# Performance work log

Hardware: AMD Instinct MI355X
Metric: run time of the kernel (lower is better)

## Reference

```python
import jax, jax.numpy as jnp
import numpy as np

B, C, Np, D = 16, 64, 128, 128
HT = 4      # time heads
HS = 4      # space heads (GAT)
F = D       # GAT out_channels
DK = D // 2 # q/k proj dim
TOPK = 8
NEG = -1e30

def ln(x, g, b):
    m = x.mean(-1, keepdims=True)
    v = jnp.mean((x - m) ** 2, axis=-1, keepdims=True)
    return (x - m) / jnp.sqrt(v + 1e-5) * g + b

def setup_inputs() -> dict:
    key = jax.random.key(0)
    ks = jax.random.split(key, 16)
    w = lambda k, s: (jax.random.normal(k, s, jnp.float32) * 0.02)
    return dict(
        H_in=jax.random.normal(ks[0], (B, C, Np, D), jnp.float32),
        static_adj=jax.random.normal(ks[1], (C, C), jnp.float32) * 0.1,
        attn_in_w=w(ks[2], (3 * D, D)), attn_in_b=jnp.zeros((3 * D,), jnp.float32),
        attn_out_w=w(ks[3], (D, D)), attn_out_b=jnp.zeros((D,), jnp.float32),
        ln1_g=jnp.ones((D,), jnp.float32), ln1_b=jnp.zeros((D,), jnp.float32),
        ln2_g=jnp.ones((D,), jnp.float32), ln2_b=jnp.zeros((D,), jnp.float32),
        ff1_w=w(ks[4], (4 * D, D)), ff1_b=jnp.zeros((4 * D,), jnp.float32),
        ff2_w=w(ks[5], (D, 4 * D)), ff2_b=jnp.zeros((D,), jnp.float32),
        tnorm_g=jnp.ones((D,), jnp.float32), tnorm_b=jnp.zeros((D,), jnp.float32),
        q_w=w(ks[6], (DK, D)), q_b=jnp.zeros((DK,), jnp.float32),
        k_w=w(ks[7], (DK, D)), k_b=jnp.zeros((DK,), jnp.float32),
        gat_w=w(ks[8], (HS, F, D)),
        gat_att_src=w(ks[9], (HS, F)), gat_att_dst=w(ks[10], (HS, F)),
        gat_bias=jnp.zeros((D,), jnp.float32),
        snorm_g=jnp.ones((D,), jnp.float32), snorm_b=jnp.zeros((D,), jnp.float32),
    )

def _forward(H_in, static_adj, attn_in_w, attn_in_b, attn_out_w, attn_out_b,
             ln1_g, ln1_b, ln2_g, ln2_b, ff1_w, ff1_b, ff2_w, ff2_b,
             tnorm_g, tnorm_b, q_w, q_b, k_w, k_b,
             gat_w, gat_att_src, gat_att_dst, gat_bias, snorm_g, snorm_b):
    dh = D // HT
    # ---- temporal transformer encoder layer (norm_first) on [B*C, Np, D]
    x0 = H_in.reshape(B * C, Np, D)
    h = ln(x0, ln1_g, ln1_b)
    qkv = h @ attn_in_w.T + attn_in_b
    q, k, v = jnp.split(qkv, 3, axis=-1)
    q = q.reshape(-1, Np, HT, dh).transpose(0, 2, 1, 3)
    k = k.reshape(-1, Np, HT, dh).transpose(0, 2, 1, 3)
    v = v.reshape(-1, Np, HT, dh).transpose(0, 2, 1, 3)
    att = jax.nn.softmax(jnp.einsum('nhqd,nhkd->nhqk', q, k) / jnp.sqrt(jnp.float32(dh)), axis=-1)
    o = jnp.einsum('nhqk,nhkd->nhqd', att, v).transpose(0, 2, 1, 3).reshape(-1, Np, D)
    x = x0 + (o @ attn_out_w.T + attn_out_b)
    h2 = ln(x, ln2_g, ln2_b)
    x = x + jax.nn.relu(h2 @ ff1_w.T + ff1_b) @ ff2_w.T + ff2_b
    H_temp = ln(x0 + x, tnorm_g, tnorm_b).reshape(B, C, Np, D)
    # ---- dynamic adjacency from temporal summary
    Hs = H_temp.mean(axis=2)                              # [B,C,D]
    q2 = Hs @ q_w.T + q_b
    k2 = Hs @ k_w.T + k_b
    sim = jnp.einsum('bcd,bed->bce', q2, k2) * (DK ** -0.5)
    A = jnp.tanh(sim) + static_adj[None]                  # [B,C,C]
    # ---- top-k edge mask per sample (row r -> its top-k cols, no self loops)
    kk = max(1, min(TOPK, C - 1))
    idx = jax.lax.top_k(A, kk)[1]                         # [B,C,kk]
    mask = jnp.any(jax.nn.one_hot(idx, C, dtype=bool), axis=2)  # [B,C,C]
    mask = mask & (~jnp.eye(C, dtype=bool)) & (A != 0)
    # ---- dense masked GAT over all (B, Np) graphs; src=row, dst=col
    xh = jnp.einsum('bcpd,hfd->bphcf', H_temp, gat_w)     # [B,Np,HS,C,F]
    asrc = jnp.einsum('bphcf,hf->bphc', xh, gat_att_src)
    adst = jnp.einsum('bphcf,hf->bphc', xh, gat_att_dst)
    e = asrc[..., :, None] + adst[..., None, :]           # [B,Np,HS,src,dst]
    e = jnp.where(e > 0, e, 0.2 * e)                      # LeakyReLU(0.2)
    mb = mask[:, None, None, :, :]
    e = jnp.where(mb, e, NEG)
    e = e - e.max(axis=3, keepdims=True)                  # softmax over src per dst
    wgt = jnp.exp(e) * mb
    s = wgt.sum(axis=3, keepdims=True)
    a = wgt / jnp.where(s > 0, s, 1.0)
    out = jnp.einsum('bphst,bphsf->bphtf', a, xh).mean(axis=2) + gat_bias  # [B,Np,C,F]
    out = out.transpose(0, 2, 1, 3)                       # [B,C,Np,D]
    return ln(out + H_temp, snorm_g, snorm_b)

def reference(H_in, static_adj, attn_in_w, attn_in_b, attn_out_w, attn_out_b,
              ln1_g, ln1_b, ln2_g, ln2_b, ff1_w, ff1_b, ff2_w, ff2_b,
              tnorm_g, tnorm_b, q_w, q_b, k_w, k_b,
              gat_w, gat_att_src, gat_att_dst, gat_bias, snorm_g, snorm_b):
    return _forward(H_in, static_adj, attn_in_w, attn_in_b, attn_out_w, attn_out_b,
                    ln1_g, ln1_b, ln2_g, ln2_b, ff1_w, ff1_b, ff2_w, ff2_b,
                    tnorm_g, tnorm_b, q_w, q_b, k_w, k_b,
                    gat_w, gat_att_src, gat_att_dst, gat_bias, snorm_g, snorm_b)
```

## Files before the change

### kernel.cpp

```cpp
#include <hip/hip_runtime.h>
#include <cstdint>


typedef __attribute__((ext_vector_type(8)))  short bf16x8;
typedef __attribute__((ext_vector_type(16))) float f32x16;
#define MFMA32(a, b, c) __builtin_amdgcn_mfma_f32_32x32x16_bf16((a), (b), (c), 0, 0, 0)

__device__ __forceinline__ unsigned short f2bf(float f) {
    unsigned int u = __float_as_uint(f);
    u += 0x7fffu + ((u >> 16) & 1u);
    return (unsigned short)(u >> 16);
}
__device__ __forceinline__ float bf2f(unsigned short u) {
    return __uint_as_float(((unsigned int)u) << 16);
}

__device__ __forceinline__ bf16x8 lds_frag(const unsigned short* p) {
    union { bf16x8 v; ushort4 h[2]; } u;
    u.h[0] = *(const ushort4*)p;
    u.h[1] = *(const ushort4*)(p + 4);
    return u.v;
}
__device__ __forceinline__ bf16x8 gfrag(const unsigned short* p) {
    union { bf16x8 v; uint4 u; } t;
    t.u = *(const uint4*)p;
    return t.v;
}

__device__ __forceinline__ int rowmap(int r, int hl) { return (r & 3) + 8 * (r >> 2) + 4 * hl; }

__device__ __forceinline__ unsigned int pk2(float lo, float hi) {
    return (unsigned int)f2bf(lo) | ((unsigned int)f2bf(hi) << 16);
}

template<int B>
__device__ __forceinline__ bf16x8 pack_frag(const f32x16& p) {
    unsigned int a0 = pk2(p[B + 0], p[B + 1]);
    unsigned int a1 = pk2(p[B + 2], p[B + 3]);
    unsigned int b0 = pk2(p[B + 4], p[B + 5]);
    unsigned int b1 = pk2(p[B + 6], p[B + 7]);
    asm("v_permlane32_swap_b32 %0, %1" : "+v"(b0), "+v"(a0));
    asm("v_permlane32_swap_b32 %0, %1" : "+v"(b1), "+v"(a1));
    union { bf16x8 v; unsigned int w[4]; } u;
    u.w[0] = a0; u.w[1] = a1; u.w[2] = b0; u.w[3] = b1;
    return u.v;
}

__global__ void wconv_kernel(const float* __restrict__ wqkv, const float* __restrict__ wout,
                             const float* __restrict__ w1, const float* __restrict__ w2,
                             const float* __restrict__ gw,
                             unsigned short* __restrict__ dst) {
    int i = blockIdx.x * 256 + threadIdx.x;
    float v;
    if (i < 49152)       v = wqkv[i];
    else if (i < 65536)  v = wout[i - 49152];
    else if (i < 131072) v = w1[i - 65536];
    else if (i < 196608) v = w2[i - 131072];
    else                 v = gw[i - 196608];
    dst[i] = f2bf(v);
}

__global__ void wa_kernel(const float* __restrict__ gw, const float* __restrict__ asw,
                          const float* __restrict__ adw,
                          float* __restrict__ waS, float* __restrict__ waD) {
    int t = blockIdx.x * 256 + threadIdx.x;
    int h = t >> 8, d = (t >> 1) & 127, which = t & 1;
    const float* av = which ? adw : asw;
    float s = 0.f;
    for (int f = 0; f < 128; f++) s += av[h * 128 + f] * gw[(h * 128 + f) * 128 + d];
    (which ? waD : waS)[h * 128 + d] = s;
}

#define QKV_STAGE(H, KBB, VTB) do {                                              \
    f32x16 accq, acck, accv;                                                     \
    _Pragma("unroll") for (int r = 0; r < 16; r++)                               \
        accq[r] = bqkv[(H) * 32 + rowmap(r, hl)];                                \
    float bk_ = bqkv[128 + (H) * 32 + l31];                                      \
    float bv_ = bqkv[256 + (H) * 32 + l31];                                      \
    _Pragma("unroll") for (int r = 0; r < 16; r++) { acck[r] = bk_; accv[r] = bv_; } \
    const unsigned short* wq_ = wqkv_b + ((H) * 32 + l31) * 128 + hl * 8;        \
    const unsigned short* wk_ = wqkv_b + (128 + (H) * 32 + l31) * 128 + hl * 8;  \
    const unsigned short* wv_ = wqkv_b + (256 + (H) * 32 + l31) * 128 + hl * 8;  \
    _Pragma("unroll") for (int k0 = 0; k0 < 128; k0 += 16) {                     \
        bf16x8 a_ = lds_frag(&RA[myrow][k0 + hl * 8]);                           \
        accq = MFMA32(gfrag(wq_ + k0), a_, accq);   \
        acck = MFMA32(a_, gfrag(wk_ + k0), acck);                                \
        accv = MFMA32(a_, gfrag(wv_ + k0), accv);                                \
    }                                                                            \
    _Pragma("unroll") for (int r = 0; r < 16; r++) {                             \
        int tok_ = wv * 32 + rowmap(r, hl);                                      \
        KBB[tok_][l31] = f2bf(acck[r]);                                          \
        VTB[l31][tok_] = f2bf(accv[r]);                                          \
    }                                                                            \
    qf0_ = pack_frag<0>(accq);                                                   \
    qf1_ = pack_frag<8>(accq);                                                   \
} while (0)

#define ATTN_PHASE(H, KBB, VTB, NEXTQKV) do {                                    \
    f32x16 sacc[4];                                                              \
    _Pragma("unroll") for (int t = 0; t < 4; t++)                                \
    _Pragma("unroll") for (int r = 0; r < 16; r++) sacc[t][r] = 0.f;             \
    _Pragma("unroll") for (int t = 0; t < 4; t++) {                              \
        bf16x8 ka0 = lds_frag(&KBB[t * 32 + l31][hl * 8]);                       \
        sacc[t] = MFMA32(ka0, qf0_, sacc[t]);                                    \
        bf16x8 ka1 = lds_frag(&KBB[t * 32 + l31][16 + hl * 8]);                  \
        sacc[t] = MFMA32(ka1, qf1_, sacc[t]);                                    \
    }                                                                            \
    NEXTQKV;                                                                     \
    const float scale_ = 0.17677669529663687f;                   \
    float m0 = -1e30f;                                                           \
    _Pragma("unroll") for (int t = 0; t < 4; t++)                                \
    _Pragma("unroll") for (int r = 0; r < 16; r++) m0 = fmaxf(m0, sacc[t][r]);   \
    m0 = fmaxf(m0, __shfl_xor(m0, 32));                                          \
    float ssum = 0.f;                                                            \
    _Pragma("unroll") for (int t = 0; t < 4; t++)                                \
    _Pragma("unroll") for (int r = 0; r < 16; r++) {                             \
        float e_ = __expf(scale_ * (sacc[t][r] - m0));                           \
        sacc[t][r] = e_; ssum += e_;                                             \
    }                                                                            \
    ssum += __shfl_xor(ssum, 32);                                                \
    float rinv_ = 1.f / ssum;                                                    \
    _Pragma("unroll") for (int t = 0; t < 4; t++)                                \
    _Pragma("unroll") for (int r = 0; r < 16; r++) sacc[t][r] *= rinv_;          \
    f32x16 oacc;                                                                 \
    _Pragma("unroll") for (int r = 0; r < 16; r++) oacc[r] = 0.f;                \
    _Pragma("unroll") for (int t = 0; t < 4; t++) {                              \
        bf16x8 pf0 = pack_frag<0>(sacc[t]);                                      \
        bf16x8 v0_ = lds_frag(&VTB[l31][t * 32 + hl * 8]);                       \
        oacc = MFMA32(pf0, v0_, oacc);                                           \
        bf16x8 pf1 = pack_frag<8>(sacc[t]);                                      \
        bf16x8 v1_ = lds_frag(&VTB[l31][t * 32 + 16 + hl * 8]);                  \
        oacc = MFMA32(pf1, v1_, oacc);                                           \
    }                                                                            \
    _Pragma("unroll") for (int j = 0; j < 8; j++)                                \
        opk[H][j] = pk2(oacc[2*j], oacc[2*j+1]);                                 \
} while (0)

__global__ __launch_bounds__(256, 2)
void temporal_kernel(const float* __restrict__ Hin,
                     const unsigned short* __restrict__ wqkv_b, const float* __restrict__ bqkv,
                     const unsigned short* __restrict__ wout_b, const float* __restrict__ bout,
                     const float* __restrict__ g1, const float* __restrict__ b1,
                     const float* __restrict__ g2, const float* __restrict__ b2,
                     const unsigned short* __restrict__ w1_b, const float* __restrict__ bf1,
                     const unsigned short* __restrict__ w2_b, const float* __restrict__ bf2,
                     const float* __restrict__ tg, const float* __restrict__ tb,
                     float* __restrict__ Htemp, float* __restrict__ Hs) {
    __shared__ unsigned short RA[128][132];
    __shared__ double RBd[4416];
    unsigned short (*kb0)[36]  = (unsigned short(*)[36])RBd;
    unsigned short (*vT0)[132] = (unsigned short(*)[132])((char*)RBd + 9216);
    unsigned short (*kb1)[36]  = (unsigned short(*)[36])((char*)RBd + 17664);
    unsigned short (*vT1)[132] = (unsigned short(*)[132])((char*)RBd + 26880);
    unsigned short (*rscr)[32][36] = (unsigned short(*)[32][36])RBd;
    float (*hsred)[128] = (float(*)[128])((char*)RBd + 9216);

    const int n = blockIdx.x;
    const int tid = threadIdx.x;
    const int lane = tid & 63;
    const int wv = tid >> 6;
    const int hl = lane >> 5;
    const int l31 = lane & 31;
    const int myrow = wv * 32 + l31;

    {
        int row = tid >> 1, hf = tid & 1;
        const float* src = Hin + ((long)n * 128 + row) * 128 + hf * 64;
        float xv[64];
        float s = 0.f, qs = 0.f;
#pragma unroll
        for (int i = 0; i < 64; i += 4) {
            float4 t = *(const float4*)(src + i);
            xv[i] = t.x; xv[i+1] = t.y; xv[i+2] = t.z; xv[i+3] = t.w;
        }
#pragma unroll
        for (int i = 0; i < 64; i++) { s += xv[i]; qs += xv[i] * xv[i]; }
        s += __shfl_xor(s, 1); qs += __shfl_xor(qs, 1);
        float mu = s * 0.0078125f;
        float rs = rsqrtf(fmaxf(qs * 0.0078125f - mu * mu, 0.f) + 1e-5f);
#pragma unroll
        for (int i = 0; i < 64; i++) {
            int d = hf * 64 + i;
            RA[row][d] = f2bf((xv[i] - mu) * rs * g1[d] + b1[d]);
        }
    }

    unsigned int opk[4][8];
    bf16x8 qf0_, qf1_;

    QKV_STAGE(0, kb0, vT0);
    __syncthreads();
    ATTN_PHASE(0, kb0, vT0, QKV_STAGE(1, kb1, vT1));
    __syncthreads();
    ATTN_PHASE(1, kb1, vT1, QKV_STAGE(2, kb0, vT0));
    __syncthreads();
    ATTN_PHASE(2, kb0, vT0, QKV_STAGE(3, kb1, vT1));
    __syncthreads();
    ATTN_PHASE(3, kb1, vT1, (void)0);

#pragma unroll
    for (int h = 0; h < 4; h++)
#pragma unroll
        for (int j = 0; j < 8; j++) {
            int tok0 = wv * 32 + rowmap(2*j,     hl);
            int tok1 = wv * 32 + rowmap(2*j + 1, hl);
            RA[tok0][h * 32 + l31] = (unsigned short)(opk[h][j] & 0xffffu);
            RA[tok1][h * 32 + l31] = (unsigned short)(opk[h][j] >> 16);
        }

    f32x16 acc[4];
#pragma unroll
    for (int t = 0; t < 4; t++) {
        float bo = bout[t * 32 + l31];
#pragma unroll
        for (int r = 0; r < 16; r++) {
            int tok = wv * 32 + rowmap(r, hl);
            acc[t][r] = Hin[((long)n * 128 + tok) * 128 + t * 32 + l31] + bo;
        }
    }
#pragma unroll
    for (int k0 = 0; k0 < 128; k0 += 16) {
        bf16x8 a = lds_frag(&RA[myrow][k0 + hl * 8]);
#pragma unroll
        for (int t = 0; t < 4; t++) {
            bf16x8 b = gfrag(wout_b + (t * 32 + l31) * 128 + k0 + hl * 8);
            acc[t] = MFMA32(a, b, acc[t]);
        }
    }

#pragma unroll
    for (int r = 0; r < 16; r++) {
        float s = acc[0][r] + acc[1][r] + acc[2][r] + acc[3][r];
#pragma unroll
        for (int d = 1; d < 32; d <<= 1) s += __shfl_xor(s, d);
        float mu = s * 0.0078125f;
        float q = 0.f;
#pragma unroll
        for (int t = 0; t < 4; t++) { float dv = acc[t][r] - mu; q += dv * dv; }
#pragma unroll
        for (int d = 1; d < 32; d <<= 1) q += __shfl_xor(q, d);
        float rs = rsqrtf(q * 0.0078125f + 1e-5f);
        int row = wv * 32 + rowmap(r, hl);
#pragma unroll
        for (int t = 0; t < 4; t++) {
            int col = t * 32 + l31;
            RA[row][col] = f2bf((acc[t][r] - mu) * rs * g2[col] + b2[col]);
        }
    }

#pragma unroll
    for (int t = 0; t < 4; t++) {
        float bv = bf2[t * 32 + l31];
#pragma unroll
        for (int r = 0; r < 16; r++) acc[t][r] += bv;
    }

    for (int j = 0; j < 4; j++) {
        f32x16 racc[4];
#pragma unroll
        for (int t = 0; t < 4; t++) {
            float bv = bf1[j * 128 + t * 32 + l31];
#pragma unroll
            for (int r = 0; r < 16; r++) racc[t][r] = bv;
        }
#pragma unroll
        for (int k0 = 0; k0 < 128; k0 += 16) {
            bf16x8 a = lds_frag(&RA[myrow][k0 + hl * 8]);
#pragma unroll
            for (int t = 0; t < 4; t++) {
                bf16x8 b = gfrag(w1_b + (j * 128 + t * 32 + l31) * 128 + k0 + hl * 8);
                racc[t] = MFMA32(a, b, racc[t]);
            }
        }
#pragma unroll
        for (int t = 0; t < 4; t++) {
#pragma unroll
            for (int r = 0; r < 16; r++)
                rscr[wv][rowmap(r, hl)][l31] = f2bf(fmaxf(racc[t][r], 0.f));
#pragma unroll
            for (int kk = 0; kk < 32; kk += 16) {
                bf16x8 a = lds_frag(&rscr[wv][l31][kk + hl * 8]);
#pragma unroll
                for (int tp = 0; tp < 4; tp++) {
                    bf16x8 b = gfrag(w2_b + (tp * 32 + l31) * 512 + j * 128 + t * 32 + kk + hl * 8);
                    acc[tp] = MFMA32(a, b, acc[tp]);
                }
            }
        }
    }

#pragma unroll
    for (int t = 0; t < 4; t++)
#pragma unroll
        for (int r = 0; r < 16; r++) {
            int tok = wv * 32 + rowmap(r, hl);
            acc[t][r] += Hin[((long)n * 128 + tok) * 128 + t * 32 + l31];
        }
    float* outf = Htemp + (long)n * 16384;
    float cs0 = 0.f, cs1 = 0.f, cs2 = 0.f, cs3 = 0.f;
#pragma unroll
    for (int r = 0; r < 16; r++) {
        float s = acc[0][r] + acc[1][r] + acc[2][r] + acc[3][r];
#pragma unroll
        for (int d = 1; d < 32; d <<= 1) s += __shfl_xor(s, d);
        float mu = s * 0.0078125f;
        float q = 0.f;
#pragma unroll
        for (int t = 0; t < 4; t++) { float dv = acc[t][r] - mu; q += dv * dv; }
#pragma unroll
        for (int d = 1; d < 32; d <<= 1) q += __shfl_xor(q, d);
        float rs = rsqrtf(q * 0.0078125f + 1e-5f);
        int tok = wv * 32 + rowmap(r, hl);
        {
            float v = (acc[0][r] - mu) * rs * tg[0 * 32 + l31] + tb[0 * 32 + l31];
            outf[tok * 128 + 0 * 32 + l31] = v;  cs0 += v;
        }
        {
            float v = (acc[1][r] - mu) * rs * tg[1 * 32 + l31] + tb[1 * 32 + l31];
            outf[tok * 128 + 1 * 32 + l31] = v;  cs1 += v;
        }
        {
            float v = (acc[2][r] - mu) * rs * tg[2 * 32 + l31] + tb[2 * 32 + l31];
            outf[tok * 128 + 2 * 32 + l31] = v;  cs2 += v;
        }
        {
            float v = (acc[3][r] - mu) * rs * tg[3 * 32 + l31] + tb[3 * 32 + l31];
            outf[tok * 128 + 3 * 32 + l31] = v;  cs3 += v;
        }
    }
    cs0 += __shfl_xor(cs0, 32); cs1 += __shfl_xor(cs1, 32);
    cs2 += __shfl_xor(cs2, 32); cs3 += __shfl_xor(cs3, 32);
    if (hl == 0) {
        hsred[wv][0 * 32 + l31] = cs0;
        hsred[wv][1 * 32 + l31] = cs1;
        hsred[wv][2 * 32 + l31] = cs2;
        hsred[wv][3 * 32 + l31] = cs3;
    }
    __syncthreads();
    if (tid < 128)
        Hs[(long)n * 128 + tid] =
            (hsred[0][tid] + hsred[1][tid] + hsred[2][tid] + hsred[3][tid]) * 0.0078125f;
}

__global__ __launch_bounds__(256)
void graph_kernel(const float* __restrict__ Hs,
                  const float* __restrict__ qw, const float* __restrict__ qb,
                  const float* __restrict__ kw, const float* __restrict__ kb,
                  const float* __restrict__ adj, unsigned long long* __restrict__ masks) {
    __shared__ float q2l[64][65];
    __shared__ float k2l[64][65];
    __shared__ float am[64][65];
    int b = blockIdx.x;
    int tid = threadIdx.x;
    {
        int r = tid & 127, jh = tid >> 7;
        int row = r & 63;
        const float* wmat = (r < 64) ? qw : kw;
        const float* bvec = (r < 64) ? qb : kb;
        const float* src = Hs + (long)(b * 64 + row) * 128;
        for (int jj = 0; jj < 32; jj++) {
            int j = jh * 32 + jj;
            const float* wrow = wmat + (long)j * 128;
            float s0 = 0.f, s1 = 0.f, s2 = 0.f, s3 = 0.f;
#pragma unroll
            for (int d = 0; d < 128; d += 4) {
                s0 += src[d] * wrow[d];     s1 += src[d+1] * wrow[d+1];
                s2 += src[d+2] * wrow[d+2]; s3 += src[d+3] * wrow[d+3];
            }
            float val = ((s0 + s1) + (s2 + s3)) + bvec[j];
            if (r < 64) q2l[row][j] = val; else k2l[row][j] = val;
        }
    }
    __syncthreads();
    {
        int c = tid & 63, eq = tid >> 6;
        for (int ee = 0; ee < 16; ee++) {
            int e = eq * 16 + ee;
            float s0 = 0.f, s1 = 0.f, s2 = 0.f, s3 = 0.f;
#pragma unroll
            for (int j = 0; j < 64; j += 4) {
                s0 += q2l[c][j]   * k2l[e][j];
                s1 += q2l[c][j+1] * k2l[e][j+1];
                s2 += q2l[c][j+2] * k2l[e][j+2];
                s3 += q2l[c][j+3] * k2l[e][j+3];
            }
            float sim = ((s0 + s1) + (s2 + s3)) * 0.125f;
            am[c][e] = tanhf(sim) + adj[c * 64 + e];
        }
    }
    __syncthreads();
    if (tid < 64) {
        int c = tid;
        unsigned long long sel = 0ull;
        for (int it = 0; it < 8; it++) {
            float best = -1e38f; int bi = 0;
            for (int e = 0; e < 64; e++) {
                float v = am[c][e];
                bool ok = (((sel >> e) & 1ull) == 0ull) && (v > best);
                best = ok ? v : best;
                bi = ok ? e : bi;
            }
            sel |= (1ull << bi);
        }
        sel &= ~(1ull << c);
        for (int e = 0; e < 64; e++)
            if (am[c][e] == 0.f) sel &= ~(1ull << e);
        masks[b * 64 + c] = sel;
    }
}

__global__ __launch_bounds__(256, 2)
void gat_kernel(float* __restrict__ Htemp,
                const unsigned short* __restrict__ gwb,
                const float* __restrict__ waS, const float* __restrict__ waD,
                const float* __restrict__ gbias,
                const unsigned long long* __restrict__ masks,
                const float* __restrict__ sg, const float* __restrict__ sb) {
    __shared__ unsigned short Htb[64][132];
    __shared__ double ovl_d[3264];
    __shared__ float asrcF[4][64], adstF[4][64];
    __shared__ float pmax[4][64], psum[4][64];
    __shared__ unsigned long long mk[64];

    unsigned short (*xhT)[68]  = (unsigned short(*)[68])ovl_d;
    unsigned short (*attT)[68] = (unsigned short(*)[68])((char*)ovl_d + 17408);
    float (*part)[8][64]       = (float(*)[8][64])ovl_d;

    const int bp = blockIdx.x;
    const int b = bp >> 7, p = bp & 127;
    const int tid = threadIdx.x;
    const int lane = tid & 63, wv = tid >> 6;
    const int hl = lane >> 5, l31 = lane & 31;
    const int rs = (wv & 1) * 32;
    const int cs = (wv >> 1) * 64;

    {
        int c = tid >> 2, qq = tid & 3;
        const float* src = Htemp + ((long)(b * 64 + c) * 128 + p) * 128 + qq * 32;
#pragma unroll
        for (int k = 0; k < 8; k++) {
            float4 t4 = *(const float4*)(src + 4 * k);
            ushort4 u; u.x = f2bf(t4.x); u.y = f2bf(t4.y); u.z = f2bf(t4.z); u.w = f2bf(t4.w);
            *(ushort4*)&Htb[c][qq * 32 + 4 * k] = u;
        }
    }
    if (tid < 64) mk[tid] = masks[b * 64 + tid];
    __syncthreads();

    {
        int s = lane, q = wv;
        float acc[8];
#pragma unroll
        for (int m = 0; m < 8; m++) acc[m] = 0.f;
        const unsigned int* hp = (const unsigned int*)&Htb[s][q * 32];
#pragma unroll
        for (int d2 = 0; d2 < 16; d2++) {
            unsigned int u = hp[d2];
            float f0 = __uint_as_float(u << 16);
            float f1 = __uint_as_float(u & 0xffff0000u);
            int d = q * 32 + 2 * d2;
#pragma unroll
            for (int h = 0; h < 4; h++) {
                acc[2*h]   += f0 * waS[h * 128 + d] + f1 * waS[h * 128 + d + 1];
                acc[2*h+1] += f0 * waD[h * 128 + d] + f1 * waD[h * 128 + d + 1];
            }
        }
#pragma unroll
        for (int m = 0; m < 8; m++) part[q][m][s] = acc[m];
    }
    __syncthreads();
    for (int o = tid; o < 512; o += 256) {
        int h = o >> 7, rem = o & 127, which = rem >> 6, s = rem & 63;
        int m = h * 2 + which;
        float v = part[0][m][s] + part[1][m][s] + part[2][m][s] + part[3][m][s];
        if (which == 0) asrcF[h][s] = v; else adstF[h][s] = v;
    }
    __syncthreads();

    f32x16 oacc0, oacc1;
#pragma unroll
    for (int r = 0; r < 16; r++) { oacc0[r] = 0.f; oacc1[r] = 0.f; }

    for (int h = 0; h < 4; h++) {
        f32x16 a0, a1;
#pragma unroll
        for (int r = 0; r < 16; r++) { a0[r] = 0.f; a1[r] = 0.f; }
        const unsigned short* gwh = gwb + h * 16384;
#pragma unroll
        for (int k0 = 0; k0 < 128; k0 += 16) {
            bf16x8 af = lds_frag(&Htb[rs + l31][k0 + hl * 8]);
            bf16x8 b0 = gfrag(gwh + (cs + l31) * 128 + k0 + hl * 8);
            bf16x8 b1 = gfrag(gwh + (cs + 32 + l31) * 128 + k0 + hl * 8);
            a0 = MFMA32(af, b0, a0);
            a1 = MFMA32(af, b1, a1);
        }
#pragma unroll
        for (int g = 0; g < 4; g++) {
            ushort4 u0, u1;
            u0.x = f2bf(a0[4*g]);   u0.y = f2bf(a0[4*g+1]);
            u0.z = f2bf(a0[4*g+2]); u0.w = f2bf(a0[4*g+3]);
            u1.x = f2bf(a1[4*g]);   u1.y = f2bf(a1[4*g+1]);
            u1.z = f2bf(a1[4*g+2]); u1.w = f2bf(a1[4*g+3]);
            int so = rs + 4 * hl + 8 * g;
            *(ushort4*)&xhT[cs + l31][so]      = u0;
            *(ushort4*)&xhT[cs + 32 + l31][so] = u1;
        }
        __syncthreads();

        {
            int t = lane;
            float adv = adstF[h][t];
            float ev[16];
            float mx = -1e30f;
#pragma unroll
            for (int i = 0; i < 16; i++) {
                int s = wv * 16 + i;
                float e = asrcF[h][s] + adv;
                e = (e > 0.f) ? e : 0.2f * e;
                ev[i] = e;
                if ((mk[s] >> t) & 1ull) mx = fmaxf(mx, e);
            }
            pmax[wv][t] = mx;
            __syncthreads();
            float M = fmaxf(fmaxf(pmax[0][t], pmax[1][t]), fmaxf(pmax[2][t], pmax[3][t]));
            float sm = 0.f;
#pragma unroll
            for (int i = 0; i < 16; i++) {
                int s = wv * 16 + i;
                float w = ((mk[s] >> t) & 1ull) ? __expf(ev[i] - M) : 0.f;
                ev[i] = w; sm += w;
            }
            psum[wv][t] = sm;
            __syncthreads();
            float S = psum[0][t] + psum[1][t] + psum[2][t] + psum[3][t];
            float rinv = (S > 0.f) ? 1.f / S : 0.f;
#pragma unroll
            for (int g = 0; g < 4; g++) {
                ushort4 u;
                u.x = f2bf(ev[4*g]   * rinv); u.y = f2bf(ev[4*g+1] * rinv);
                u.z = f2bf(ev[4*g+2] * rinv); u.w = f2bf(ev[4*g+3] * rinv);
                *(ushort4*)&attT[t][wv * 16 + 4 * g] = u;
            }
        }
        __syncthreads();

#pragma unroll
        for (int k0 = 0; k0 < 64; k0 += 16) {
            bf16x8 af = lds_frag(&attT[rs + l31][k0 + hl * 8]);
            bf16x8 b0 = lds_frag(&xhT[cs + l31][k0 + hl * 8]);
            bf16x8 b1 = lds_frag(&xhT[cs + 32 + l31][k0 + hl * 8]);
            oacc0 = MFMA32(af, b0, oacc0);
            oacc1 = MFMA32(af, b1, oacc1);
        }
        __syncthreads();
    }

    float gb0 = gbias[cs + l31], gb1 = gbias[cs + 32 + l31];
    float v0[16], v1[16];
#pragma unroll
    for (int r = 0; r < 16; r++) {
        int c = rs + rowmap(r, hl);
        v0[r] = oacc0[r] * 0.25f + gb0 + bf2f(Htb[c][cs + l31]);
        v1[r] = oacc1[r] * 0.25f + gb1 + bf2f(Htb[c][cs + 32 + l31]);
    }
#pragma unroll
    for (int r = 0; r < 16; r++) {
        float s = v0[r] + v1[r];
        float q = v0[r] * v0[r] + v1[r] * v1[r];
#pragma unroll
        for (int d = 1; d < 32; d <<= 1) { s += __shfl_xor(s, d); q += __shfl_xor(q, d); }
        if (l31 == 0) {
            int c = rs + rowmap(r, hl);
            pmax[wv >> 1][c] = s;
            psum[wv >> 1][c] = q;
        }
    }
    __syncthreads();
    float sgv0 = sg[cs + l31], sbv0 = sb[cs + l31];
    float sgv1 = sg[cs + 32 + l31], sbv1 = sb[cs + 32 + l31];
#pragma unroll
    for (int r = 0; r < 16; r++) {
        int c = rs + rowmap(r, hl);
        float sum = pmax[0][c] + pmax[1][c];
        float sq  = psum[0][c] + psum[1][c];
        float mu = sum * 0.0078125f;
        float var = sq * 0.0078125f - mu * mu;
        float rsd = rsqrtf(fmaxf(var, 0.f) + 1e-5f);
        float* orow = Htemp + ((long)(b * 64 + c) * 128 + p) * 128;
        orow[cs + l31]      = (v0[r] - mu) * rsd * sgv0 + sbv0;
        orow[cs + 32 + l31] = (v1[r] - mu) * rsd * sgv1 + sbv1;
    }
}

extern "C" void kernel_launch(void* const* d_in, const int* in_sizes, int n_in,
                              void* d_out, int out_size, void* d_ws, size_t ws_size,
                              hipStream_t stream) {
    const float* Hin        = (const float*)d_in[0];
    const float* static_adj = (const float*)d_in[1];
    const float* attn_in_w  = (const float*)d_in[2];
    const float* attn_in_b  = (const float*)d_in[3];
    const float* attn_out_w = (const float*)d_in[4];
    const float* attn_out_b = (const float*)d_in[5];
    const float* ln1_g      = (const float*)d_in[6];
    const float* ln1_b      = (const float*)d_in[7];
    const float* ln2_g      = (const float*)d_in[8];
    const float* ln2_b      = (const float*)d_in[9];
    const float* ff1_w      = (const float*)d_in[10];
    const float* ff1_b      = (const float*)d_in[11];
    const float* ff2_w      = (const float*)d_in[12];
    const float* ff2_b      = (const float*)d_in[13];
    const float* tnorm_g    = (const float*)d_in[14];
    const float* tnorm_b    = (const float*)d_in[15];
    const float* q_w        = (const float*)d_in[16];
    const float* q_b        = (const float*)d_in[17];
    const float* k_w        = (const float*)d_in[18];
    const float* k_b        = (const float*)d_in[19];
    const float* gat_w      = (const float*)d_in[20];
    const float* gat_att_src= (const float*)d_in[21];
    const float* gat_att_dst= (const float*)d_in[22];
    const float* gat_bias   = (const float*)d_in[23];
    const float* snorm_g    = (const float*)d_in[24];
    const float* snorm_b    = (const float*)d_in[25];

    float* out = (float*)d_out;
    char* ws = (char*)d_ws;
    unsigned short* wb = (unsigned short*)ws;
    const unsigned short* wqkv_b = wb;
    const unsigned short* wout_b = wb + 49152;
    const unsigned short* w1_b   = wb + 65536;
    const unsigned short* w2_b   = wb + 131072;
    const unsigned short* gw_b   = wb + 196608;
    unsigned long long* masks = (unsigned long long*)(ws + 524288);
    float* Hs  = (float*)(ws + 532480);
    float* waS = (float*)(ws + 1056768);
    float* waD = (float*)(ws + 1058816);

    hipLaunchKernelGGL(wconv_kernel, dim3(1024), dim3(256), 0, stream,
                       attn_in_w, attn_out_w, ff1_w, ff2_w, gat_w, wb);
    hipLaunchKernelGGL(wa_kernel, dim3(4), dim3(256), 0, stream,
                       gat_w, gat_att_src, gat_att_dst, waS, waD);
    hipLaunchKernelGGL(temporal_kernel, dim3(1024), dim3(256), 0, stream,
                       Hin, wqkv_b, attn_in_b, wout_b, attn_out_b,
                       ln1_g, ln1_b, ln2_g, ln2_b,
                       w1_b, ff1_b, w2_b, ff2_b, tnorm_g, tnorm_b, out, Hs);
    hipLaunchKernelGGL(graph_kernel, dim3(16), dim3(256), 0, stream,
                       Hs, q_w, q_b, k_w, k_b, static_adj, masks);
    hipLaunchKernelGGL(gat_kernel, dim3(2048), dim3(256), 0, stream,
                       out, gw_b, waS, waD, gat_bias,
                       masks, snorm_g, snorm_b);
}
```

Baseline: 552.9 us.

## Double-buffer GAT head projections and compute softmax weights in registers as MFMA operands

```diff
diff --git a/kernel.cpp b/kernel.cpp
--- a/kernel.cpp
+++ b/kernel.cpp
@@ -409,6 +409,64 @@
     }
 }
 
+#define XH_STAGE(H, XT) do {                                                     \
+    f32x16 a0_, a1_;                                                             \
+    _Pragma("unroll") for (int r = 0; r < 16; r++) { a0_[r] = 0.f; a1_[r] = 0.f; } \
+    const unsigned short* gwh_ = gwb + (H) * 16384;                              \
+    _Pragma("unroll") for (int k0 = 0; k0 < 128; k0 += 16) {                     \
+        bf16x8 af_ = lds_frag(&Htb[rs + l31][k0 + hl * 8]);                      \
+        bf16x8 b0_ = gfrag(gwh_ + (cs + l31) * 128 + k0 + hl * 8);               \
+        bf16x8 b1_ = gfrag(gwh_ + (cs + 32 + l31) * 128 + k0 + hl * 8);          \
+        a0_ = MFMA32(af_, b0_, a0_);                                             \
+        a1_ = MFMA32(af_, b1_, a1_);                                             \
+    }                                                                            \
+    _Pragma("unroll") for (int g = 0; g < 4; g++) {                              \
+        ushort4 u0_, u1_;                                                        \
+        u0_.x = f2bf(a0_[4*g]);   u0_.y = f2bf(a0_[4*g+1]);                      \
+        u0_.z = f2bf(a0_[4*g+2]); u0_.w = f2bf(a0_[4*g+3]);                      \
+        u1_.x = f2bf(a1_[4*g]);   u1_.y = f2bf(a1_[4*g+1]);                      \
+        u1_.z = f2bf(a1_[4*g+2]); u1_.w = f2bf(a1_[4*g+3]);                      \
+        int so_ = rs + 4 * hl + 8 * g;                                           \
+        *(ushort4*)&XT[cs + l31][so_]      = u0_;                                \
+        *(ushort4*)&XT[cs + 32 + l31][so_] = u1_;                                \
+    }                                                                            \
+} while (0)
+
+#define PV_PHASE(H, XT, NEXTXH) do {                                             \
+    float adv_ = adstF[H][rs + l31];                    \
+    float ev_[4][8];                                                             \
+    float M_ = -1e30f;                                                           \
+    _Pragma("unroll") for (int q = 0; q < 4; q++)                                \
+    _Pragma("unroll") for (int j = 0; j < 8; j++) {                              \
+        int s_ = q * 16 + hl * 8 + j;                                            \
+        float e_ = asrcF[H][s_] + adv_;                                          \
+        e_ = (e_ > 0.f) ? e_ : 0.2f * e_;                                        \
+        ev_[q][j] = e_;                                                          \
+        if ((mt >> s_) & 1ull) M_ = fmaxf(M_, e_);                               \
+    }                                                                            \
+    M_ = fmaxf(M_, __shfl_xor(M_, 32));                                          \
+    float sm_ = 0.f;                                                             \
+    _Pragma("unroll") for (int q = 0; q < 4; q++)                                \
+    _Pragma("unroll") for (int j = 0; j < 8; j++) {                              \
+        int s_ = q * 16 + hl * 8 + j;                                            \
+        float w_ = ((mt >> s_) & 1ull) ? __expf(ev_[q][j] - M_) : 0.f;           \
+        ev_[q][j] = w_; sm_ += w_;                                               \
+    }                                                                            \
+    sm_ += __shfl_xor(sm_, 32);                                                  \
+    float rinv_ = (sm_ > 0.f) ? 1.f / sm_ : 0.f;                                 \
+    NEXTXH;                                                                      \
+    _Pragma("unroll") for (int q = 0; q < 4; q++) {                              \
+        union { bf16x8 v; unsigned int w[4]; } uu_;                              \
+        uu_.w[0] = pk2(ev_[q][0] * rinv_, ev_[q][1] * rinv_);                    \
+        uu_.w[1] = pk2(ev_[q][2] * rinv_, ev_[q][3] * rinv_);                    \
+        uu_.w[2] = pk2(ev_[q][4] * rinv_, ev_[q][5] * rinv_);                    \
+        uu_.w[3] = pk2(ev_[q][6] * rinv_, ev_[q][7] * rinv_);                    \
+        bf16x8 af_ = uu_.v;                                                      \
+        oacc0 = MFMA32(af_, lds_frag(&XT[cs + l31][q * 16 + hl * 8]), oacc0);    \
+        oacc1 = MFMA32(af_, lds_frag(&XT[cs + 32 + l31][q * 16 + hl * 8]), oacc1); \
+    }                                                                            \
+} while (0)
+
 __global__ __launch_bounds__(256, 2)
 void gat_kernel(float* __restrict__ Htemp,
                 const unsigned short* __restrict__ gwb,
@@ -417,14 +475,16 @@
                 const unsigned long long* __restrict__ masks,
                 const float* __restrict__ sg, const float* __restrict__ sb) {
     __shared__ unsigned short Htb[64][132];
-    __shared__ double ovl_d[3264];
+    __shared__ double xbuf0[2176];
+    __shared__ double xbuf1[2176];
     __shared__ float asrcF[4][64], adstF[4][64];
-    __shared__ float pmax[4][64], psum[4][64];
+    __shared__ float pr0[2][64], pr1[2][64];
     __shared__ unsigned long long mk[64];
-
-    unsigned short (*xhT)[68]  = (unsigned short(*)[68])ovl_d;
-    unsigned short (*attT)[68] = (unsigned short(*)[68])((char*)ovl_d + 17408);
-    float (*part)[8][64]       = (float(*)[8][64])ovl_d;
+    __shared__ unsigned long long mTT[64];
+
+    unsigned short (*xhT0)[68] = (unsigned short(*)[68])xbuf0;
+    unsigned short (*xhT1)[68] = (unsigned short(*)[68])xbuf1;
+    float (*part)[8][64]       = (float(*)[8][64])xbuf0;
 
     const int bp = blockIdx.x;
     const int b = bp >> 7, p = bp & 127;
@@ -475,85 +535,29 @@
         float v = part[0][m][s] + part[1][m][s] + part[2][m][s] + part[3][m][s];
         if (which == 0) asrcF[h][s] = v; else adstF[h][s] = v;
     }
-    __syncthreads();
+    if (tid < 64) {
+        unsigned long long m = 0ull;
+        for (int s = 0; s < 64; s++)
+            m |= ((mk[s] >> tid) & 1ull) << s;
+        mTT[tid] = m;
+    }
+    __syncthreads();
+
+    const unsigned long long mt = mTT[rs + l31];
 
     f32x16 oacc0, oacc1;
 #pragma unroll
     for (int r = 0; r < 16; r++) { oacc0[r] = 0.f; oacc1[r] = 0.f; }
 
-    for (int h = 0; h < 4; h++) {
-        f32x16 a0, a1;
-#pragma unroll
-        for (int r = 0; r < 16; r++) { a0[r] = 0.f; a1[r] = 0.f; }
-        const unsigned short* gwh = gwb + h * 16384;
-#pragma unroll
-        for (int k0 = 0; k0 < 128; k0 += 16) {
-            bf16x8 af = lds_frag(&Htb[rs + l31][k0 + hl * 8]);
-            bf16x8 b0 = gfrag(gwh + (cs + l31) * 128 + k0 + hl * 8);
-            bf16x8 b1 = gfrag(gwh + (cs + 32 + l31) * 128 + k0 + hl * 8);
-            a0 = MFMA32(af, b0, a0);
-            a1 = MFMA32(af, b1, a1);
-        }
-#pragma unroll
-        for (int g = 0; g < 4; g++) {
-            ushort4 u0, u1;
-            u0.x = f2bf(a0[4*g]);   u0.y = f2bf(a0[4*g+1]);
-            u0.z = f2bf(a0[4*g+2]); u0.w = f2bf(a0[4*g+3]);
-            u1.x = f2bf(a1[4*g]);   u1.y = f2bf(a1[4*g+1]);
-            u1.z = f2bf(a1[4*g+2]); u1.w = f2bf(a1[4*g+3]);
-            int so = rs + 4 * hl + 8 * g;
-            *(ushort4*)&xhT[cs + l31][so]      = u0;
-            *(ushort4*)&xhT[cs + 32 + l31][so] = u1;
-        }
-        __syncthreads();
-
-        {
-            int t = lane;
-            float adv = adstF[h][t];
-            float ev[16];
-            float mx = -1e30f;
-#pragma unroll
-            for (int i = 0; i < 16; i++) {
-                int s = wv * 16 + i;
-                float e = asrcF[h][s] + adv;
-                e = (e > 0.f) ? e : 0.2f * e;
-                ev[i] = e;
-                if ((mk[s] >> t) & 1ull) mx = fmaxf(mx, e);
-            }
-            pmax[wv][t] = mx;
-            __syncthreads();
-            float M = fmaxf(fmaxf(pmax[0][t], pmax[1][t]), fmaxf(pmax[2][t], pmax[3][t]));
-            float sm = 0.f;
-#pragma unroll
-            for (int i = 0; i < 16; i++) {
-                int s = wv * 16 + i;
-                float w = ((mk[s] >> t) & 1ull) ? __expf(ev[i] - M) : 0.f;
-                ev[i] = w; sm += w;
-            }
-            psum[wv][t] = sm;
-            __syncthreads();
-            float S = psum[0][t] + psum[1][t] + psum[2][t] + psum[3][t];
-            float rinv = (S > 0.f) ? 1.f / S : 0.f;
-#pragma unroll
-            for (int g = 0; g < 4; g++) {
-                ushort4 u;
-                u.x = f2bf(ev[4*g]   * rinv); u.y = f2bf(ev[4*g+1] * rinv);
-                u.z = f2bf(ev[4*g+2] * rinv); u.w = f2bf(ev[4*g+3] * rinv);
-                *(ushort4*)&attT[t][wv * 16 + 4 * g] = u;
-            }
-        }
-        __syncthreads();
-
-#pragma unroll
-        for (int k0 = 0; k0 < 64; k0 += 16) {
-            bf16x8 af = lds_frag(&attT[rs + l31][k0 + hl * 8]);
-            bf16x8 b0 = lds_frag(&xhT[cs + l31][k0 + hl * 8]);
-            bf16x8 b1 = lds_frag(&xhT[cs + 32 + l31][k0 + hl * 8]);
-            oacc0 = MFMA32(af, b0, oacc0);
-            oacc1 = MFMA32(af, b1, oacc1);
-        }
-        __syncthreads();
-    }
+    XH_STAGE(0, xhT0);
+    __syncthreads();
+    PV_PHASE(0, xhT0, XH_STAGE(1, xhT1));
+    __syncthreads();
+    PV_PHASE(1, xhT1, XH_STAGE(2, xhT0));
+    __syncthreads();
+    PV_PHASE(2, xhT0, XH_STAGE(3, xhT1));
+    __syncthreads();
+    PV_PHASE(3, xhT1, (void)0);
 
     float gb0 = gbias[cs + l31], gb1 = gbias[cs + 32 + l31];
     float v0[16], v1[16];
@@ -571,8 +575,8 @@
         for (int d = 1; d < 32; d <<= 1) { s += __shfl_xor(s, d); q += __shfl_xor(q, d); }
         if (l31 == 0) {
             int c = rs + rowmap(r, hl);
-            pmax[wv >> 1][c] = s;
-            psum[wv >> 1][c] = q;
+            pr0[wv >> 1][c] = s;
+            pr1[wv >> 1][c] = q;
         }
     }
     __syncthreads();
@@ -581,8 +585,8 @@
 #pragma unroll
     for (int r = 0; r < 16; r++) {
         int c = rs + rowmap(r, hl);
-        float sum = pmax[0][c] + pmax[1][c];
-        float sq  = psum[0][c] + psum[1][c];
+        float sum = pr0[0][c] + pr0[1][c];
+        float sq  = pr1[0][c] + pr1[1][c];
         float mu = sum * 0.0078125f;
         float var = sq * 0.0078125f - mu * mu;
         float rsd = rsqrtf(fmaxf(var, 0.f) + 1e-5f);
```

Result: slower. 567.1 us (+2.6%).

## Store temporal output as transposed bf16 for GAT, merge weight prep kernels

Applied to the files above, without the earlier changes.

```diff
diff --git a/kernel.cpp b/kernel.cpp
--- a/kernel.cpp
+++ b/kernel.cpp
@@ -46,29 +46,29 @@
     return u.v;
 }
 
-__global__ void wconv_kernel(const float* __restrict__ wqkv, const float* __restrict__ wout,
-                             const float* __restrict__ w1, const float* __restrict__ w2,
-                             const float* __restrict__ gw,
-                             unsigned short* __restrict__ dst) {
-    int i = blockIdx.x * 256 + threadIdx.x;
-    float v;
-    if (i < 49152)       v = wqkv[i];
-    else if (i < 65536)  v = wout[i - 49152];
-    else if (i < 131072) v = w1[i - 65536];
-    else if (i < 196608) v = w2[i - 131072];
-    else                 v = gw[i - 196608];
-    dst[i] = f2bf(v);
-}
-
-__global__ void wa_kernel(const float* __restrict__ gw, const float* __restrict__ asw,
-                          const float* __restrict__ adw,
-                          float* __restrict__ waS, float* __restrict__ waD) {
-    int t = blockIdx.x * 256 + threadIdx.x;
-    int h = t >> 8, d = (t >> 1) & 127, which = t & 1;
-    const float* av = which ? adw : asw;
-    float s = 0.f;
-    for (int f = 0; f < 128; f++) s += av[h * 128 + f] * gw[(h * 128 + f) * 128 + d];
-    (which ? waD : waS)[h * 128 + d] = s;
+__global__ void prep_kernel(const float* __restrict__ wqkv, const float* __restrict__ wout,
+                            const float* __restrict__ w1, const float* __restrict__ w2,
+                            const float* __restrict__ gw,
+                            const float* __restrict__ asw, const float* __restrict__ adw,
+                            unsigned short* __restrict__ dst,
+                            float* __restrict__ waS, float* __restrict__ waD) {
+    if (blockIdx.x < 1024) {
+        int i = blockIdx.x * 256 + threadIdx.x;
+        float v;
+        if (i < 49152)       v = wqkv[i];
+        else if (i < 65536)  v = wout[i - 49152];
+        else if (i < 131072) v = w1[i - 65536];
+        else if (i < 196608) v = w2[i - 131072];
+        else                 v = gw[i - 196608];
+        dst[i] = f2bf(v);
+    } else {
+        int t = (blockIdx.x - 1024) * 256 + threadIdx.x;
+        int h = t >> 8, d = (t >> 1) & 127, which = t & 1;
+        const float* av = which ? adw : asw;
+        float s = 0.f;
+        for (int f = 0; f < 128; f++) s += av[h * 128 + f] * gw[(h * 128 + f) * 128 + d];
+        (which ? waD : waS)[h * 128 + d] = s;
+    }
 }
 
 #define QKV_STAGE(H, KBB, VTB) do {                                              \
@@ -136,6 +136,7 @@
         opk[H][j] = pk2(oacc[2*j], oacc[2*j+1]);                                 \
 } while (0)
 
+template<int BF16>
 __global__ __launch_bounds__(256, 2)
 void temporal_kernel(const float* __restrict__ Hin,
                      const unsigned short* __restrict__ wqkv_b, const float* __restrict__ bqkv,
@@ -145,7 +146,8 @@
                      const unsigned short* __restrict__ w1_b, const float* __restrict__ bf1,
                      const unsigned short* __restrict__ w2_b, const float* __restrict__ bf2,
                      const float* __restrict__ tg, const float* __restrict__ tb,
-                     float* __restrict__ Htemp, float* __restrict__ Hs) {
+                     float* __restrict__ Htemp, float* __restrict__ Hs,
+                     unsigned short* __restrict__ hbt) {
     __shared__ unsigned short RA[128][132];
     __shared__ double RBd[4416];
     unsigned short (*kb0)[36]  = (unsigned short(*)[36])RBd;
@@ -296,6 +298,7 @@
             int tok = wv * 32 + rowmap(r, hl);
             acc[t][r] += Hin[((long)n * 128 + tok) * 128 + t * 32 + l31];
         }
+    const int bb = n >> 6, cc = n & 63;
     float* outf = Htemp + (long)n * 16384;
     float cs0 = 0.f, cs1 = 0.f, cs2 = 0.f, cs3 = 0.f;
 #pragma unroll
@@ -311,21 +314,22 @@
         for (int d = 1; d < 32; d <<= 1) q += __shfl_xor(q, d);
         float rs = rsqrtf(q * 0.0078125f + 1e-5f);
         int tok = wv * 32 + rowmap(r, hl);
-        {
-            float v = (acc[0][r] - mu) * rs * tg[0 * 32 + l31] + tb[0 * 32 + l31];
-            outf[tok * 128 + 0 * 32 + l31] = v;  cs0 += v;
-        }
-        {
-            float v = (acc[1][r] - mu) * rs * tg[1 * 32 + l31] + tb[1 * 32 + l31];
-            outf[tok * 128 + 1 * 32 + l31] = v;  cs1 += v;
-        }
-        {
-            float v = (acc[2][r] - mu) * rs * tg[2 * 32 + l31] + tb[2 * 32 + l31];
-            outf[tok * 128 + 2 * 32 + l31] = v;  cs2 += v;
-        }
-        {
-            float v = (acc[3][r] - mu) * rs * tg[3 * 32 + l31] + tb[3 * 32 + l31];
-            outf[tok * 128 + 3 * 32 + l31] = v;  cs3 += v;
+        float v0 = (acc[0][r] - mu) * rs * tg[0 * 32 + l31] + tb[0 * 32 + l31];
+        float v1 = (acc[1][r] - mu) * rs * tg[1 * 32 + l31] + tb[1 * 32 + l31];
+        float v2 = (acc[2][r] - mu) * rs * tg[2 * 32 + l31] + tb[2 * 32 + l31];
+        float v3 = (acc[3][r] - mu) * rs * tg[3 * 32 + l31] + tb[3 * 32 + l31];
+        cs0 += v0; cs1 += v1; cs2 += v2; cs3 += v3;
+        if constexpr (BF16) {
+            unsigned short* ob = hbt + ((long)(bb * 128 + tok) * 64 + cc) * 128 + l31;
+            ob[0]  = f2bf(v0);
+            ob[32] = f2bf(v1);
+            ob[64] = f2bf(v2);
+            ob[96] = f2bf(v3);
+        } else {
+            outf[tok * 128 + 0 * 32 + l31] = v0;
+            outf[tok * 128 + 1 * 32 + l31] = v1;
+            outf[tok * 128 + 2 * 32 + l31] = v2;
+            outf[tok * 128 + 3 * 32 + l31] = v3;
         }
     }
     cs0 += __shfl_xor(cs0, 32); cs1 += __shfl_xor(cs1, 32);
@@ -409,8 +413,10 @@
     }
 }
 
+template<int BF16>
 __global__ __launch_bounds__(256, 2)
 void gat_kernel(float* __restrict__ Htemp,
+                const unsigned short* __restrict__ hbt,
                 const unsigned short* __restrict__ gwb,
                 const float* __restrict__ waS, const float* __restrict__ waD,
                 const float* __restrict__ gbias,
@@ -434,7 +440,13 @@
     const int rs = (wv & 1) * 32;
     const int cs = (wv >> 1) * 64;
 
-    {
+    if constexpr (BF16) {
+        int c = tid >> 2, qq = tid & 3;
+        const unsigned short* src = hbt + ((long)(b * 128 + p) * 64 + c) * 128 + qq * 32;
+#pragma unroll
+        for (int m = 0; m < 8; m++)
+            *(ushort4*)&Htb[c][qq * 32 + 4 * m] = *(const ushort4*)(src + 4 * m);
+    } else {
         int c = tid >> 2, qq = tid & 3;
         const float* src = Htemp + ((long)(b * 64 + c) * 128 + p) * 128 + qq * 32;
 #pragma unroll
@@ -634,18 +646,31 @@
     float* Hs  = (float*)(ws + 532480);
     float* waS = (float*)(ws + 1056768);
     float* waD = (float*)(ws + 1058816);
-
-    hipLaunchKernelGGL(wconv_kernel, dim3(1024), dim3(256), 0, stream,
-                       attn_in_w, attn_out_w, ff1_w, ff2_w, gat_w, wb);
-    hipLaunchKernelGGL(wa_kernel, dim3(4), dim3(256), 0, stream,
-                       gat_w, gat_att_src, gat_att_dst, waS, waD);
-    hipLaunchKernelGGL(temporal_kernel, dim3(1024), dim3(256), 0, stream,
-                       Hin, wqkv_b, attn_in_b, wout_b, attn_out_b,
-                       ln1_g, ln1_b, ln2_g, ln2_b,
-                       w1_b, ff1_b, w2_b, ff2_b, tnorm_g, tnorm_b, out, Hs);
-    hipLaunchKernelGGL(graph_kernel, dim3(16), dim3(256), 0, stream,
-                       Hs, q_w, q_b, k_w, k_b, static_adj, masks);
-    hipLaunchKernelGGL(gat_kernel, dim3(2048), dim3(256), 0, stream,
-                       out, gw_b, waS, waD, gat_bias,
-                       masks, snorm_g, snorm_b);
-}
+    unsigned short* hbt = (unsigned short*)(ws + 1060864);
+    const bool big_ws = ws_size >= (size_t)(1060864 + 33554432);
+
+    hipLaunchKernelGGL(prep_kernel, dim3(1028), dim3(256), 0, stream,
+                       attn_in_w, attn_out_w, ff1_w, ff2_w, gat_w,
+                       gat_att_src, gat_att_dst, wb, waS, waD);
+    if (big_ws) {
+        hipLaunchKernelGGL((temporal_kernel<1>), dim3(1024), dim3(256), 0, stream,
+                           Hin, wqkv_b, attn_in_b, wout_b, attn_out_b,
+                           ln1_g, ln1_b, ln2_g, ln2_b,
+                           w1_b, ff1_b, w2_b, ff2_b, tnorm_g, tnorm_b, out, Hs, hbt);
+        hipLaunchKernelGGL(graph_kernel, dim3(16), dim3(256), 0, stream,
+                           Hs, q_w, q_b, k_w, k_b, static_adj, masks);
+        hipLaunchKernelGGL((gat_kernel<1>), dim3(2048), dim3(256), 0, stream,
+                           out, hbt, gw_b, waS, waD, gat_bias,
+                           masks, snorm_g, snorm_b);
+    } else {
+        hipLaunchKernelGGL((temporal_kernel<0>), dim3(1024), dim3(256), 0, stream,
+                           Hin, wqkv_b, attn_in_b, wout_b, attn_out_b,
+                           ln1_g, ln1_b, ln2_g, ln2_b,
+                           w1_b, ff1_b, w2_b, ff2_b, tnorm_g, tnorm_b, out, Hs, hbt);
+        hipLaunchKernelGGL(graph_kernel, dim3(16), dim3(256), 0, stream,
+                           Hs, q_w, q_b, k_w, k_b, static_adj, masks);
+        hipLaunchKernelGGL((gat_kernel<0>), dim3(2048), dim3(256), 0, stream,
+                           out, hbt, gw_b, waS, waD, gat_bias,
+                           masks, snorm_g, snorm_b);
+    }
+}
```

Result: faster. 537.6 us (-2.8%).
